# Kernel optimization log

Measured on AMD Instinct MI355X. Metric: run time of the kernel, lower is better.

## Reference

```python
import jax, jax.numpy as jnp
import numpy as np

B, N, C = 2, 2048, 1024
H, D = 16, 64
SEQ_DROPOUT = 0.4
K_KEEP = int(N * (1.0 - SEQ_DROPOUT))  # 1228 kept keys per (b, h)


def setup_inputs() -> dict:
    key = jax.random.key(0)
    k1, k2, k3, k4, k5 = jax.random.split(key, 5)
    x = jax.random.normal(k1, (B, N, C), dtype=jnp.float32)
    W_qkv = jax.random.normal(k2, (3 * H * D, C), dtype=jnp.float32) * 0.02
    W_out = jax.random.normal(k3, (C, H * D), dtype=jnp.float32) * 0.02
    pos_bias = jax.random.normal(k4, (H, N, N), dtype=jnp.float32) * 0.1
    seq_mask = jax.random.randint(k5, (B, H, N), 0, 10, dtype=jnp.int32)
    mask = jnp.zeros((B, N), dtype=bool)  # True = padded / masked out
    return {"x": x, "W_qkv": W_qkv, "W_out": W_out, "pos_bias": pos_bias,
            "seq_mask": seq_mask, "mask": mask}


def reference(x, W_qkv, W_out, pos_bias, seq_mask, mask):
    scale = D ** -0.5
    # qkv projection: (b n (h d qkv)) -> q,k,v each [B,H,N,D]
    qkv = (x @ W_qkv.T).reshape(B, N, H, D, 3)
    q = jnp.moveaxis(qkv[..., 0], 2, 1)
    k_full = jnp.moveaxis(qkv[..., 1], 2, 1)
    v_full = jnp.moveaxis(qkv[..., 2], 2, 1)

    # random top-k key subsampling per (b, h); padded positions forced out
    sm = jnp.where(mask[:, None, :], jnp.int32(-1), seq_mask)
    _, idx = jax.lax.top_k(sm, K_KEEP)              # [B,H,K]
    idx = jnp.sort(idx, axis=-1)

    kk = jnp.take_along_axis(k_full, idx[..., None], axis=2)  # [B,H,K,D]
    vv = jnp.take_along_axis(v_full, idx[..., None], axis=2)
    k_mask = jnp.take_along_axis(jnp.broadcast_to(mask[:, None, :], (B, H, N)), idx, axis=-1)

    dots = jnp.einsum('bhid,bhjd->bhij', q, kk) * scale       # [B,H,N,K]
    # gather position bias columns at kept key indices
    pb = jnp.take_along_axis(pos_bias[None], idx[:, :, None, :], axis=-1)  # [B,H,N,K]
    dots = dots + pb

    qk_mask = jnp.logical_and(mask[:, None, :, None], k_mask[:, :, None, :])
    causal = idx[:, :, None, :] > jnp.arange(N)[None, None, :, None]
    qk_mask = jnp.logical_or(qk_mask, causal)

    dots = jnp.where(qk_mask, -jnp.finfo(dots.dtype).max, dots)
    attn = jax.nn.softmax(dots, axis=-1)
    out = jnp.einsum('bhij,bhjd->bhid', attn, vv)             # [B,H,N,D]
    out = jnp.moveaxis(out, 1, 2).reshape(B, N, H * D)
    return out @ W_out.T
```

## Files before the change

kernel.cpp:

```cpp
#include <hip/hip_runtime.h>
#include <hip/hip_bf16.h>
#include <float.h>

#define BB    2
#define NSEQ  2048
#define CDIM  1024
#define HH    16
#define DD    64
#define KKEEP 1228

typedef __attribute__((ext_vector_type(8))) short short8_t;
typedef __attribute__((ext_vector_type(4))) short short4_t;
typedef __attribute__((ext_vector_type(4))) float f32x4;
typedef __attribute__((ext_vector_type(16))) float f32x16;
typedef __attribute__((ext_vector_type(4))) float float4_t;
typedef __attribute__((ext_vector_type(4))) unsigned uint4_t;
typedef __bf16 bf16x8 __attribute__((ext_vector_type(8)));

#define Z16 ((f32x16){0.f,0.f,0.f,0.f,0.f,0.f,0.f,0.f,0.f,0.f,0.f,0.f,0.f,0.f,0.f,0.f})

static __device__ __forceinline__ short f2bf(float x) {
  __hip_bfloat16 h = __float2bfloat16(x);
  short s;
  __builtin_memcpy(&s, &h, 2);
  return s;
}

static __device__ __forceinline__ float bf2f(short s) {
  unsigned u = ((unsigned)(unsigned short)s) << 16;
  float f;
  __builtin_memcpy(&f, &u, 4);
  return f;
}

static __device__ __forceinline__ f32x4 mfma16(bf16x8 a, bf16x8 b, f32x4 c) {
  return __builtin_amdgcn_mfma_f32_16x16x32_bf16(a, b, c, 0, 0, 0);
}

static __device__ __forceinline__ f32x16 mfma32(bf16x8 a, bf16x8 b, f32x16 c) {
  return __builtin_amdgcn_mfma_f32_32x32x16_bf16(a, b, c, 0, 0, 0);
}

static __device__ __forceinline__ void gll16(const void* g, void* l) {
  __builtin_amdgcn_global_load_lds((const __attribute__((address_space(1))) void*)g,
                                   (__attribute__((address_space(3))) void*)l,
                                   16, 0, 0);
}

static __device__ __forceinline__ int soff(int tau) {
  if (tau == 0) return 0;
  if (tau < 32) return 4 + (tau - 1) * 2;
  if (tau < 48) return 66 + (tau - 32) * 3;
  return 114 + (tau - 48) * 4;
}
#define SLOTS_PER_BH 178

__global__ __launch_bounds__(256) void cast_f32_bf16_kernel(
    const float* __restrict__ src, short* __restrict__ dst, int n4) {
  int i = blockIdx.x * 256 + threadIdx.x;
  if (i >= n4) return;
  float4_t v = ((const float4_t*)src)[i];
  short4_t o;
  o[0] = f2bf(v[0]); o[1] = f2bf(v[1]); o[2] = f2bf(v[2]); o[3] = f2bf(v[3]);
  ((short4_t*)dst)[i] = o;
}

__global__ __launch_bounds__(256) void cast_wqkv_kernel(
    const float* __restrict__ w, short* __restrict__ dst) {
  int rr = blockIdx.x;
  int c = rr >> 10, hd = rr & 1023;
  int h = hd >> 6, d = hd & 63;
  int srow = h * 192 + d * 3 + c;
  int col = threadIdx.x * 4;
  float4_t v = *(const float4_t*)(w + (size_t)srow * CDIM + col);
  short4_t o;
  o[0] = f2bf(v[0]); o[1] = f2bf(v[1]); o[2] = f2bf(v[2]); o[3] = f2bf(v[3]);
  *(short4_t*)(dst + (size_t)rr * CDIM + col) = o;
}

template <int EPI>
__global__ __launch_bounds__(256) void gemm_bt_kernel(
    const short* __restrict__ A, const short* __restrict__ B, int K, int N,
    float* __restrict__ outF, short* __restrict__ outQ,
    short* __restrict__ outK, short* __restrict__ outV) {
  __shared__ __align__(16) short lA[128 * 32];
  __shared__ __align__(16) short lB[128 * 32];
  int m0 = blockIdx.y * 128, n0 = blockIdx.x * 128;
  int tid = threadIdx.x, lane = tid & 63;
  int w = tid >> 6;
  int lq = lane & 15, lg = lane >> 4;
  int wm = w >> 1, wn = w & 1;

  f32x4 acc[4][4];
#pragma unroll
  for (int m = 0; m < 4; ++m)
#pragma unroll
    for (int n = 0; n < 4; ++n) acc[m][n] = (f32x4){0.f, 0.f, 0.f, 0.f};

  const int c0 = tid, c1 = tid + 256;
  const short* Ar0 = A + (size_t)(m0 + (c0 >> 2)) * K + (c0 & 3) * 8;
  const short* Ar1 = A + (size_t)(m0 + (c1 >> 2)) * K + (c1 & 3) * 8;
  const short* Br0 = B + (size_t)(n0 + (c0 >> 2)) * K + (c0 & 3) * 8;
  const short* Br1 = B + (size_t)(n0 + (c1 >> 2)) * K + (c1 & 3) * 8;

  for (int k0 = 0; k0 < K; k0 += 32) {
    gll16(Ar0 + k0, lA + c0 * 8);
    gll16(Ar1 + k0, lA + c1 * 8);
    gll16(Br0 + k0, lB + c0 * 8);
    gll16(Br1 + k0, lB + c1 * 8);
    __syncthreads();
    bf16x8 af[4], bf[4];
#pragma unroll
    for (int m = 0; m < 4; ++m)
      af[m] = *(const bf16x8*)(lA + (wm * 64 + m * 16 + lq) * 32 + lg * 8);
#pragma unroll
    for (int n = 0; n < 4; ++n)
      bf[n] = *(const bf16x8*)(lB + (wn * 64 + n * 16 + lq) * 32 + lg * 8);
#pragma unroll
    for (int m = 0; m < 4; ++m)
#pragma unroll
      for (int n = 0; n < 4; ++n) acc[m][n] = mfma16(af[m], bf[n], acc[m][n]);
    __syncthreads();
  }

#pragma unroll
  for (int m = 0; m < 4; ++m)
#pragma unroll
    for (int n = 0; n < 4; ++n) {
      int row_b = m0 + wm * 64 + m * 16 + lg * 4;
      int col = n0 + wn * 64 + n * 16 + lq;
#pragma unroll
      for (int r = 0; r < 4; ++r) {
        float v = acc[m][n][r];
        int row = row_b + r;
        if constexpr (EPI == 1) {
          outF[(size_t)row * N + col] = v;
        } else {
          int c = col >> 10, cc = col & 1023;
          int bb2 = row >> 11, nn = row & 2047;
          int hh2 = cc >> 6, dd2 = cc & 63;
          int bh = bb2 * HH + hh2;
          short val = f2bf(v);
          if (c == 0) {
            outQ[((size_t)bh * NSEQ + nn) * DD + dd2] = val;
          } else if (c == 1) {
            int t = nn >> 5, s = dd2 >> 4;
            int lane2 = (nn & 31) | ((dd2 & 8) << 2);
            outK[(((size_t)bh * 64 + t) * 4 + s) * 512 + lane2 * 8 + (dd2 & 7)] = val;
          } else {
            int t = nn >> 5;
            int c4 = (dd2 >> 5) * 2 + ((nn >> 4) & 1);
            int lane2 = (dd2 & 31) | ((nn & 8) << 2);
            outV[(((size_t)bh * 64 + t) * 4 + c4) * 512 + lane2 * 8 + (nn & 7)] = val;
          }
        }
      }
    }
}

__global__ __launch_bounds__(256) void topk_kernel(const int* __restrict__ seq_mask,
                                                   unsigned* __restrict__ keepw,
                                                   int* __restrict__ jminb) {
  __shared__ int hist[10];
  __shared__ int vals[NSEQ];
  __shared__ int seqc[256];
  __shared__ unsigned wbuf[64];
  __shared__ int sT, sNeed, sMin;
  int bh = blockIdx.x, tid = threadIdx.x;
  if (tid < 10) hist[tid] = 0;
  if (tid < 64) wbuf[tid] = 0;
  if (tid == 0) sMin = NSEQ;
  __syncthreads();
  const int* sm = seq_mask + (size_t)bh * NSEQ;
  for (int i = tid; i < NSEQ; i += 256) {
    int v = sm[i];
    vals[i] = v;
    atomicAdd(&hist[v], 1);
  }
  __syncthreads();
  if (tid == 0) {
    int cum = 0, t = 0;
    for (int v = 9; v >= 0; --v) {
      int hv = hist[v];
      if (cum + hv >= KKEEP) { t = v; break; }
      cum += hv;
    }
    sT = t;
    sNeed = KKEEP - cum;
  }
  __syncthreads();
  int t = sT, need = sNeed;
  int base = tid * 8, leq = 0;
  int lv[8];
#pragma unroll
  for (int j = 0; j < 8; ++j) {
    lv[j] = vals[base + j];
    leq += (lv[j] == t);
  }
  seqc[tid] = leq;
  __syncthreads();
  for (int off = 1; off < 256; off <<= 1) {
    int a = 0;
    if (tid >= off) a = seqc[tid - off];
    __syncthreads();
    seqc[tid] += a;
    __syncthreads();
  }
  int eqp = seqc[tid] - leq;
  unsigned mybits = 0;
#pragma unroll
  for (int j = 0; j < 8; ++j) {
    int v = lv[j];
    bool kept = (v > t) || (v == t && eqp < need);
    if (v == t) eqp++;
    if (kept) mybits |= (1u << j);
  }
  atomicOr(&wbuf[tid >> 2], mybits << ((tid & 3) * 8));
  if (mybits) atomicMin(&sMin, base + __ffs(mybits) - 1);
  __syncthreads();
  if (tid < 64) keepw[(size_t)bh * 64 + tid] = wbuf[tid];
  if (tid == 0) jminb[bh] = sMin;
}

#define PBLOAD(SUF, T)                                                         \
  do {                                                                         \
    const float* pb_ = pbrow + (T) * 32 + hi4;                                 \
    pbg0##SUF = *(const float4_t*)(pb_);                                       \
    pbg1##SUF = *(const float4_t*)(pb_ + 8);                                   \
    pbg2##SUF = *(const float4_t*)(pb_ + 16);                                  \
    pbg3##SUF = *(const float4_t*)(pb_ + 24);                                  \
    kw##SUF = kwp[T];                                                          \
  } while (0)

#define CHUNK32(SUF, OSUF, T)                                                  \
  do {                                                                         \
    int kb0c = (T) * 32;                                                       \
    const short* kc_ = pkb + (size_t)(T) * 2048 + lane * 8;                    \
    bf16x8 k0 = *(const bf16x8*)(kc_);                                         \
    bf16x8 k1 = *(const bf16x8*)(kc_ + 512);                                   \
    bf16x8 k2 = *(const bf16x8*)(kc_ + 1024);                                  \
    bf16x8 k3 = *(const bf16x8*)(kc_ + 1536);                                  \
    const short* vc_ = pvb + (size_t)(T) * 2048 + lane * 8;                    \
    bf16x8 v00 = *(const bf16x8*)(vc_);                                        \
    bf16x8 v01 = *(const bf16x8*)(vc_ + 512);                                  \
    bf16x8 v10 = *(const bf16x8*)(vc_ + 1024);                                 \
    bf16x8 v11 = *(const bf16x8*)(vc_ + 1536);                                 \
    if ((T) + 1 < t1) PBLOAD(OSUF, (T) + 1);                                   \
    f32x16 s = Z16;                                                            \
    s = mfma32(k0, qf0, s);                                                    \
    s = mfma32(k1, qf1, s);                                                    \
    s = mfma32(k2, qf2, s);                                                    \
    s = mfma32(k3, qf3, s);                                                    \
    float sv[16];                                                              \
    unsigned vb = 0;                                                           \
    float cm = -FLT_MAX;                                                       \
    _Pragma("unroll") for (int g = 0; g < 4; ++g) {                            \
      float4_t pbg = (g == 0) ? pbg0##SUF : (g == 1) ? pbg1##SUF               \
                   : (g == 2) ? pbg2##SUF : pbg3##SUF;                         \
      _Pragma("unroll") for (int m = 0; m < 4; ++m) {                          \
        int rr = g * 4 + m;                                                    \
        int kk = m + g * 8 + hi4;                                              \
        int jj = kb0c + kk;                                                    \
        unsigned keep = (kw##SUF >> kk) & 1u;                                  \
        float x = (keep && jj <= qglob) ? fmaf(s[rr], 0.125f, pbg[m])          \
                                        : -FLT_MAX;                            \
        vb |= keep << rr;                                                      \
        sv[rr] = x;                                                            \
        cm = fmaxf(cm, x);                                                     \
      }                                                                        \
    }                                                                          \
    if (__any(cm > mrun)) {                     \
      float rm = fmaxf(cm, __shfl_xor(cm, 32));                                \
      float mnew = fmaxf(mrun, rm);                                            \
      float fsc = __expf(mrun - mnew);                                         \
      mrun = mnew;                                                             \
      lsum *= fsc;                                                             \
      _Pragma("unroll") for (int rr = 0; rr < 16; ++rr) {                      \
        int qr = (rr & 3) + 8 * (rr >> 2) + hi4;                               \
        float fr = __shfl(fsc, qr);                                            \
        o0[rr] *= fr;                                                          \
        o1[rr] *= fr;                                                          \
      }                                                                        \
    }                                                                          \
    float pv[16];                                                              \
    float psum = 0.f;                                                          \
    _Pragma("unroll") for (int rr = 0; rr < 16; ++rr) {                        \
      float p_ = ((vb >> rr) & 1u) ? __expf(sv[rr] - mrun) : 0.f;              \
      pv[rr] = p_;                                                             \
      psum += p_;                                                              \
    }                                                                          \
    lsum += psum;                                                              \
    unsigned w0_, w1_, w2_, w3_, w4_, w5_, w6_, w7_;                           \
    asm("v_cvt_pk_bf16_f32 %0, %1, %2" : "=v"(w0_) : "v"(pv[0]), "v"(pv[1]));  \
    asm("v_cvt_pk_bf16_f32 %0, %1, %2" : "=v"(w1_) : "v"(pv[2]), "v"(pv[3]));  \
    asm("v_cvt_pk_bf16_f32 %0, %1, %2" : "=v"(w2_) : "v"(pv[4]), "v"(pv[5]));  \
    asm("v_cvt_pk_bf16_f32 %0, %1, %2" : "=v"(w3_) : "v"(pv[6]), "v"(pv[7]));  \
    asm("v_cvt_pk_bf16_f32 %0, %1, %2" : "=v"(w4_) : "v"(pv[8]), "v"(pv[9]));  \
    asm("v_cvt_pk_bf16_f32 %0, %1, %2" : "=v"(w5_) : "v"(pv[10]), "v"(pv[11]));\
    asm("v_cvt_pk_bf16_f32 %0, %1, %2" : "=v"(w6_) : "v"(pv[12]), "v"(pv[13]));\
    asm("v_cvt_pk_bf16_f32 %0, %1, %2" : "=v"(w7_) : "v"(pv[14]), "v"(pv[15]));\
    asm("v_permlane32_swap_b32 %0, %1" : "+v"(w0_), "+v"(w2_));                \
    asm("v_permlane32_swap_b32 %0, %1" : "+v"(w1_), "+v"(w3_));                \
    asm("v_permlane32_swap_b32 %0, %1" : "+v"(w4_), "+v"(w6_));                \
    asm("v_permlane32_swap_b32 %0, %1" : "+v"(w5_), "+v"(w7_));                \
    uint4_t u0_ = {w0_, w1_, w2_, w3_};                                        \
    uint4_t u1_ = {w4_, w5_, w6_, w7_};                                        \
    bf16x8 pf0 = __builtin_bit_cast(bf16x8, u0_);                              \
    bf16x8 pf1 = __builtin_bit_cast(bf16x8, u1_);                              \
    o0 = mfma32(pf0, v00, o0);                                                 \
    o0 = mfma32(pf1, v01, o0);                                                 \
    o1 = mfma32(pf0, v10, o1);                                                 \
    o1 = mfma32(pf1, v11, o1);                                                 \
  } while (0)

__global__ __launch_bounds__(128) void attn_split_kernel(
    const short* __restrict__ qb, const short* __restrict__ PK,
    const short* __restrict__ PV, const unsigned* __restrict__ keepw,
    const int* __restrict__ jminb, const float* __restrict__ pos_bias,
    short* __restrict__ Opart, float* __restrict__ mlb) {
  int w = threadIdx.x >> 6, lane = threadIdx.x & 63;
  int lq32 = lane & 31, hi = lane >> 5;
  int hi4 = hi * 4, hi8 = hi * 8;
  int gid = blockIdx.x * 2 + w;
  int bh = gid & 31;
  int r = gid >> 5;
  int tau, part;
  if (r < 64)       { tau = 63 - (r >> 2); part = r & 3; }
  else if (r < 112) { int rr = r - 64; tau = 47 - rr / 3; part = rr % 3; }
  else if (r < 116) { tau = 0; part = r - 112; }
  else              { int rr = r - 116; tau = 31 - (rr >> 1); part = rr & 1; }
  int P = (tau == 0 || tau >= 48) ? 4 : (tau >= 32) ? 3 : 2;

  int h = bh & 15;
  int q0 = tau << 5;
  int qglob = q0 + lq32;
  int jmin = jminb[bh];
  int nkb = (q0 < jmin) ? 64 : (tau + 1);
  int t0 = (nkb * part) / P, t1 = (nkb * (part + 1)) / P;

  const short* qp_ = qb + ((size_t)bh * NSEQ + qglob) * DD + hi8;
  bf16x8 qf0 = *(const bf16x8*)(qp_);
  bf16x8 qf1 = *(const bf16x8*)(qp_ + 16);
  bf16x8 qf2 = *(const bf16x8*)(qp_ + 32);
  bf16x8 qf3 = *(const bf16x8*)(qp_ + 48);

  const short* pkb = PK + (size_t)bh * 131072;
  const short* pvb = PV + (size_t)bh * 131072;
  const float* pbrow = pos_bias + ((size_t)h * NSEQ + qglob) * NSEQ;
  const unsigned* kwp = keepw + (size_t)bh * 64;

  float mrun = -FLT_MAX, lsum = 0.f;
  f32x16 o0 = Z16, o1 = Z16;

  float4_t pbg0A, pbg1A, pbg2A, pbg3A, pbg0B, pbg1B, pbg2B, pbg3B;
  unsigned kwA, kwB;

  if (t0 < t1) {
    PBLOAD(A, t0);
    int t = t0;
    for (;;) {
      CHUNK32(A, B, t);
      if (++t >= t1) break;
      CHUNK32(B, A, t);
      if (++t >= t1) break;
    }
  }

  float ltot = lsum + __shfl_xor(lsum, 32);

  int sidx = bh * SLOTS_PER_BH + soff(tau) + part;
  if (hi == 0) {
    mlb[(size_t)sidx * 64 + lq32] = mrun;
    mlb[(size_t)sidx * 64 + 32 + lq32] = ltot;
  }
  short* op = Opart + (size_t)sidx * 2048;
#pragma unroll
  for (int rr = 0; rr < 16; ++rr) {
    int qr = (rr & 3) + 8 * (rr >> 2) + hi4;
    op[qr * 64 + lq32]      = f2bf(o0[rr]);
    op[qr * 64 + 32 + lq32] = f2bf(o1[rr]);
  }
}

__global__ __launch_bounds__(64) void combine_kernel(
    const float* __restrict__ mlb, const short* __restrict__ Opart,
    short* __restrict__ attn_out) {
  int blk = blockIdx.x;
  int bh = blk & 31, tau = blk >> 5;
  int P = (tau == 0 || tau >= 48) ? 4 : (tau >= 32) ? 3 : 2;
  int s0 = bh * SLOTS_PER_BH + soff(tau);
  int b = bh >> 4, h = bh & 15;
  int lane = threadIdx.x;
  int q = lane >> 1, d0 = (lane & 1) * 32;

  float m[4], l[4];
  float M = -FLT_MAX;
  for (int p = 0; p < P; ++p) {
    m[p] = mlb[(size_t)(s0 + p) * 64 + q];
    l[p] = mlb[(size_t)(s0 + p) * 64 + 32 + q];
    M = fmaxf(M, m[p]);
  }
  float f[4];
  float L = 0.f;
  for (int p = 0; p < P; ++p) {
    f[p] = __expf(m[p] - M);
    L += l[p] * f[p];
  }
  float inv = 1.f / L;

  short* orow = attn_out + ((size_t)b * NSEQ + tau * 32 + q) * CDIM + h * DD + d0;
#pragma unroll
  for (int c = 0; c < 4; ++c) {
    float acc[8] = {0.f, 0.f, 0.f, 0.f, 0.f, 0.f, 0.f, 0.f};
    for (int p = 0; p < P; ++p) {
      short8_t x = *(const short8_t*)(Opart + (size_t)(s0 + p) * 2048 + q * 64 + d0 + c * 8);
#pragma unroll
      for (int jj = 0; jj < 8; ++jj) acc[jj] += f[p] * bf2f(x[jj]);
    }
    short8_t oo;
#pragma unroll
    for (int jj = 0; jj < 8; ++jj) oo[jj] = f2bf(acc[jj] * inv);
    *(short8_t*)(orow + c * 8) = oo;
  }
}

extern "C" void kernel_launch(void* const* d_in, const int* in_sizes, int n_in,
                              void* d_out, int out_size, void* d_ws, size_t ws_size,
                              hipStream_t stream) {
  const float* x        = (const float*)d_in[0];
  const float* Wqkv     = (const float*)d_in[1];
  const float* Wout     = (const float*)d_in[2];
  const float* pos_bias = (const float*)d_in[3];
  const int*   seq_mask = (const int*)d_in[4];
  float* out = (float*)d_out;

  char* ws = (char*)d_ws;
  short* qb    = (short*)(ws);
  short* PK    = (short*)(ws + ((size_t)8  << 20));
  short* PV    = (short*)(ws + ((size_t)16 << 20));
  short* woutb = (short*)(ws + ((size_t)24 << 20));
  short* xb    = (short*)(ws + ((size_t)26 << 20));
  short* wqkvb = (short*)(ws + ((size_t)34 << 20));
  short* Opart = (short*)(ws + ((size_t)26 << 20));
  float* mlb   = (float*)(ws + ((size_t)495 << 17));
  short* aob   = (short*)(ws + ((size_t)51 << 20));
  unsigned* keepw = (unsigned*)(ws + ((size_t)59 << 20) + (512 << 10));
  int* jminb   = (int*)(ws + ((size_t)59 << 20) + (512 << 10) + 65536);

  cast_f32_bf16_kernel<<<4096, 256, 0, stream>>>(x, xb, (BB * NSEQ * CDIM) / 4);
  cast_wqkv_kernel<<<3072, 256, 0, stream>>>(Wqkv, wqkvb);
  cast_f32_bf16_kernel<<<1024, 256, 0, stream>>>(Wout, woutb, (CDIM * HH * DD) / 4);

  gemm_bt_kernel<0><<<dim3(24, 32), 256, 0, stream>>>(xb, wqkvb, CDIM, 3 * HH * DD,
                                                      nullptr, qb, PK, PV);

  topk_kernel<<<BB * HH, 256, 0, stream>>>(seq_mask, keepw, jminb);

  attn_split_kernel<<<2848, 128, 0, stream>>>(qb, PK, PV, keepw, jminb,
                                              pos_bias, Opart, mlb);

  combine_kernel<<<2048, 64, 0, stream>>>(mlb, Opart, aob);

  gemm_bt_kernel<1><<<dim3(8, 32), 256, 0, stream>>>(aob, woutb, HH * DD, CDIM,
                                                     out, nullptr, nullptr, nullptr);
}
```

Baseline: 178.7 us.

## Share pos_bias tiles across batches via LDS double buffering

The attention kernel now maps both batch elements for the same head and query tile onto the two waves of one block. The pos_bias tile is loaded once into double-buffered shared memory and read by both waves, instead of each wave loading it separately from global memory. This halves global pos_bias traffic, which is the dominant stream. In exchange it adds a __syncthreads per chunk, and the key-block range now uses the larger jmin across the two batches, so one wave may process extra fully masked blocks.

```diff
diff --git a/kernel.cpp b/kernel.cpp
--- a/kernel.cpp
+++ b/kernel.cpp
@@ -11,6 +11,7 @@
 
 typedef __attribute__((ext_vector_type(8))) short short8_t;
 typedef __attribute__((ext_vector_type(4))) short short4_t;
+typedef __attribute__((ext_vector_type(2))) float float2_t;
 typedef __attribute__((ext_vector_type(4))) float f32x4;
 typedef __attribute__((ext_vector_type(16))) float f32x16;
 typedef __attribute__((ext_vector_type(4))) float float4_t;
@@ -222,17 +223,7 @@
   if (tid == 0) jminb[bh] = sMin;
 }
 
-#define PBLOAD(SUF, T)                                                         \
-  do {                                                                         \
-    const float* pb_ = pbrow + (T) * 32 + hi4;                                 \
-    pbg0##SUF = *(const float4_t*)(pb_);                                       \
-    pbg1##SUF = *(const float4_t*)(pb_ + 8);                                   \
-    pbg2##SUF = *(const float4_t*)(pb_ + 16);                                  \
-    pbg3##SUF = *(const float4_t*)(pb_ + 24);                                  \
-    kw##SUF = kwp[T];                                                          \
-  } while (0)
-
-#define CHUNK32(SUF, OSUF, T)                                                  \
+#define CHUNK32(T, BUF)                                                        \
   do {                                                                         \
     int kb0c = (T) * 32;                                                       \
     const short* kc_ = pkb + (size_t)(T) * 2048 + lane * 8;                    \
@@ -245,7 +236,7 @@
     bf16x8 v01 = *(const bf16x8*)(vc_ + 512);                                  \
     bf16x8 v10 = *(const bf16x8*)(vc_ + 1024);                                 \
     bf16x8 v11 = *(const bf16x8*)(vc_ + 1536);                                 \
-    if ((T) + 1 < t1) PBLOAD(OSUF, (T) + 1);                                   \
+    unsigned kw = kwp[T];                                                      \
     f32x16 s = Z16;                                                            \
     s = mfma32(k0, qf0, s);                                                    \
     s = mfma32(k1, qf1, s);                                                    \
@@ -255,14 +246,16 @@
     unsigned vb = 0;                                                           \
     float cm = -FLT_MAX;                                                       \
     _Pragma("unroll") for (int g = 0; g < 4; ++g) {                            \
-      float4_t pbg = (g == 0) ? pbg0##SUF : (g == 1) ? pbg1##SUF               \
-                   : (g == 2) ? pbg2##SUF : pbg3##SUF;                         \
+      float2_t pA_ = *(const float2_t*)&ls[BUF][lq32][g * 8 + hi4];            \
+      float2_t pB_ = *(const float2_t*)&ls[BUF][lq32][g * 8 + hi4 + 2];        \
       _Pragma("unroll") for (int m = 0; m < 4; ++m) {                          \
         int rr = g * 4 + m;                                                    \
         int kk = m + g * 8 + hi4;                                              \
         int jj = kb0c + kk;                                                    \
-        unsigned keep = (kw##SUF >> kk) & 1u;                                  \
-        float x = (keep && jj <= qglob) ? fmaf(s[rr], 0.125f, pbg[m])          \
+        float pbv = (m == 0) ? pA_[0] : (m == 1) ? pA_[1]                      \
+                  : (m == 2) ? pB_[0] : pB_[1];                                \
+        unsigned keep = (kw >> kk) & 1u;                                       \
+        float x = (keep && jj <= qglob) ? fmaf(s[rr], 0.125f, pbv)             \
                                         : -FLT_MAX;                            \
         vb |= keep << rr;                                                      \
         sv[rr] = x;                                                            \
@@ -318,12 +311,14 @@
     const short* __restrict__ PV, const unsigned* __restrict__ keepw,
     const int* __restrict__ jminb, const float* __restrict__ pos_bias,
     short* __restrict__ Opart, float* __restrict__ mlb) {
-  int w = threadIdx.x >> 6, lane = threadIdx.x & 63;
+  __shared__ float ls[2][32][34];
+  int tid = threadIdx.x;
+  int w = tid >> 6, lane = tid & 63;
   int lq32 = lane & 31, hi = lane >> 5;
   int hi4 = hi * 4, hi8 = hi * 8;
-  int gid = blockIdx.x * 2 + w;
-  int bh = gid & 31;
-  int r = gid >> 5;
+  int blk = blockIdx.x;
+  int h = blk & 15;
+  int r = blk >> 4;
   int tau, part;
   if (r < 64)       { tau = 63 - (r >> 2); part = r & 3; }
   else if (r < 112) { int rr = r - 64; tau = 47 - rr / 3; part = rr % 3; }
@@ -331,11 +326,12 @@
   else              { int rr = r - 116; tau = 31 - (rr >> 1); part = rr & 1; }
   int P = (tau == 0 || tau >= 48) ? 4 : (tau >= 32) ? 3 : 2;
 
-  int h = bh & 15;
+  int bh = w * HH + h;
   int q0 = tau << 5;
   int qglob = q0 + lq32;
-  int jmin = jminb[bh];
-  int nkb = (q0 < jmin) ? 64 : (tau + 1);
+  int jm0 = jminb[h], jm1 = jminb[HH + h];
+  int jmx = (jm0 > jm1) ? jm0 : jm1;
+  int nkb = (q0 < jmx) ? 64 : (tau + 1);
   int t0 = (nkb * part) / P, t1 = (nkb * (part + 1)) / P;
 
   const short* qp_ = qb + ((size_t)bh * NSEQ + qglob) * DD + hi8;
@@ -346,23 +342,44 @@
 
   const short* pkb = PK + (size_t)bh * 131072;
   const short* pvb = PV + (size_t)bh * 131072;
-  const float* pbrow = pos_bias + ((size_t)h * NSEQ + qglob) * NSEQ;
   const unsigned* kwp = keepw + (size_t)bh * 64;
+
+  int srow = tid >> 2, scol = (tid & 3) * 8;
+  const float* pbsrc = pos_bias + ((size_t)h * NSEQ + q0 + srow) * NSEQ + scol;
 
   float mrun = -FLT_MAX, lsum = 0.f;
   f32x16 o0 = Z16, o1 = Z16;
 
-  float4_t pbg0A, pbg1A, pbg2A, pbg3A, pbg0B, pbg1B, pbg2B, pbg3B;
-  unsigned kwA, kwB;
-
   if (t0 < t1) {
-    PBLOAD(A, t0);
-    int t = t0;
+    {
+      float4_t ra0 = *(const float4_t*)(pbsrc + (size_t)t0 * 32);
+      float4_t ra1 = *(const float4_t*)(pbsrc + (size_t)t0 * 32 + 4);
+      float* lp = &ls[0][srow][scol];
+      *(float2_t*)(lp + 0) = (float2_t){ra0[0], ra0[1]};
+      *(float2_t*)(lp + 2) = (float2_t){ra0[2], ra0[3]};
+      *(float2_t*)(lp + 4) = (float2_t){ra1[0], ra1[1]};
+      *(float2_t*)(lp + 6) = (float2_t){ra1[2], ra1[3]};
+    }
+    int t = t0, buf = 0;
     for (;;) {
-      CHUNK32(A, B, t);
-      if (++t >= t1) break;
-      CHUNK32(B, A, t);
-      if (++t >= t1) break;
+      bool more = (t + 1 < t1);
+      float4_t rb0, rb1;
+      if (more) {
+        rb0 = *(const float4_t*)(pbsrc + (size_t)(t + 1) * 32);
+        rb1 = *(const float4_t*)(pbsrc + (size_t)(t + 1) * 32 + 4);
+      }
+      __syncthreads();
+      CHUNK32(t, buf);
+      if (more) {
+        float* lp = &ls[buf ^ 1][srow][scol];
+        *(float2_t*)(lp + 0) = (float2_t){rb0[0], rb0[1]};
+        *(float2_t*)(lp + 2) = (float2_t){rb0[2], rb0[3]};
+        *(float2_t*)(lp + 4) = (float2_t){rb1[0], rb1[1]};
+        *(float2_t*)(lp + 6) = (float2_t){rb1[2], rb1[3]};
+      }
+      ++t;
+      if (t >= t1) break;
+      buf ^= 1;
     }
   }
 
```

Result: no change. 177.1 us (-0.9%).
